# Kernel tuning notes

Measured on AMD Instinct MI355X. Metric: run time of the kernel, lower is better.

## Reference

```python
import jax, jax.numpy as jnp
import numpy as np

N, E, D = 100000, 1600000, 128


def setup_inputs() -> dict:
    key = jax.random.key(0)
    ks = jax.random.split(key, 8)
    s = 1.0 / np.sqrt(D)
    return {
        "x": jax.random.normal(ks[0], (N, D), dtype=jnp.float32),
        "edge_index": jax.random.randint(ks[1], (2, E), 0, N, dtype=jnp.int64),
        "x_prev": jax.random.normal(ks[2], (N, D), dtype=jnp.float32),
        # GCNConv params: weight [in,out], bias [out]
        "W": jax.random.uniform(ks[3], (D, D), jnp.float32, -s, s),
        "b": jnp.zeros((D,), jnp.float32),
        # GRUCell params (torch layout): [3*H, H] gates ordered (r, z, n)
        "W_ih": jax.random.uniform(ks[4], (3 * D, D), jnp.float32, -s, s),
        "W_hh": jax.random.uniform(ks[5], (3 * D, D), jnp.float32, -s, s),
        "b_ih": jax.random.uniform(ks[6], (3 * D,), jnp.float32, -s, s),
        "b_hh": jax.random.uniform(ks[7], (3 * D,), jnp.float32, -s, s),
    }


def _gcn_conv(x, edge_index, W, b):
    n = x.shape[0]
    loop = jnp.arange(n, dtype=edge_index.dtype)
    src = jnp.concatenate([edge_index[0], loop])  # [E+N]
    dst = jnp.concatenate([edge_index[1], loop])
    # symmetric normalization: deg over destinations (incl. self loops)
    deg = jax.ops.segment_sum(jnp.ones_like(dst, dtype=x.dtype), dst, num_segments=n)
    dinv = jnp.where(deg > 0, jax.lax.rsqrt(deg), 0.0)
    norm = dinv[src] * dinv[dst]  # [E+N]
    xw = x @ W  # [N, out]
    msg = xw[src] * norm[:, None]  # gather + scale
    return jax.ops.segment_sum(msg, dst, num_segments=n) + b


def _gru_cell(inp, h, W_ih, W_hh, b_ih, b_hh):
    gi = inp @ W_ih.T + b_ih  # [N, 3H]
    gh = h @ W_hh.T + b_hh
    i_r, i_z, i_n = jnp.split(gi, 3, axis=-1)
    h_r, h_z, h_n = jnp.split(gh, 3, axis=-1)
    r = jax.nn.sigmoid(i_r + h_r)
    z = jax.nn.sigmoid(i_z + h_z)
    ntil = jnp.tanh(i_n + r * h_n)
    return (1.0 - z) * ntil + z * h


def reference(x, edge_index, x_prev, W, b, W_ih, W_hh, b_ih, b_hh):
    h_cur = _gcn_conv(x, edge_index, W, b)
    return _gru_cell(h_cur, x_prev, W_ih, W_hh, b_ih, b_hh)
```

## Files before the change

### kernel.cpp

```cpp
#include <hip/hip_runtime.h>
#include <hip/hip_bf16.h>
#include <math.h>

#define DIM 128
#define PSHIFT 10
#define PSZ 1024
#define CHUNK 2048

typedef __attribute__((ext_vector_type(8))) short bf16x8;
typedef __attribute__((ext_vector_type(4))) float f32x4;
typedef unsigned short u16;
typedef unsigned int u32;
typedef unsigned long long u64;

__device__ __forceinline__ u16 f2bf(float x) {
    u32 u = __builtin_bit_cast(u32, x);
    u += 0x7fff + ((u >> 16) & 1);
    return (u16)(u >> 16);
}
__device__ __forceinline__ float bf2f(u16 h) {
    return __builtin_bit_cast(float, (u32)h << 16);
}
__device__ __forceinline__ float fsig(float x) {
    return __builtin_amdgcn_rcpf(1.f + __expf(-x));
}
__device__ __forceinline__ float ftanh(float x) {
    return 1.f - 2.f * __builtin_amdgcn_rcpf(__expf(2.f * x) + 1.f);
}


__global__ __launch_bounds__(256) void k_zero(int* __restrict__ p, int n) {
    int i = blockIdx.x * 256 + threadIdx.x;
    if (i < n) p[i] = 0;
}

__global__ __launch_bounds__(256) void k_pcount(const int* __restrict__ edst,
                                                int* __restrict__ pcnt, int E) {
    __shared__ int h[128];
    int t = threadIdx.x;
    if (t < 128) h[t] = 0;
    __syncthreads();
    int stride = gridDim.x * 256;
    for (int e = blockIdx.x * 256 + t; e < E; e += stride)
        atomicAdd(&h[edst[e] >> PSHIFT], 1);
    __syncthreads();
    if (t < 128 && h[t]) atomicAdd(&pcnt[t], h[t]);
}

__global__ __launch_bounds__(256) void k_pscan(const int* __restrict__ pcnt,
                                               int* __restrict__ poff,
                                               int* __restrict__ pfill,
                                               int* __restrict__ rowp,
                                               int P, int N, int E) {
    __shared__ int a[256];
    int t = threadIdx.x;
    int v = (t < P) ? pcnt[t] : 0;
    a[t] = v;
    __syncthreads();
    #pragma unroll
    for (int off = 1; off < 256; off <<= 1) {
        int y = (t >= off) ? a[t - off] : 0;
        __syncthreads();
        a[t] += y;
        __syncthreads();
    }
    int excl = a[t] - v;
    if (t < P) { poff[t] = excl; pfill[t] = excl; }
    if (t == 0) { poff[P] = E; rowp[N] = E; }
}

__global__ __launch_bounds__(256) void k_pscatter(const int* __restrict__ esrc,
                                                  const int* __restrict__ edst,
                                                  int* __restrict__ pfill,
                                                  u64* __restrict__ pbuf, int E) {
    __shared__ int hist[128], sc[128], lofs[128], gbase[128];
    __shared__ u32 ss[CHUNK], sd[CHUNK];
    int t = threadIdx.x;
    int c0 = blockIdx.x * CHUNK;
    int cnt = E - c0; if (cnt > CHUNK) cnt = CHUNK;

    if (t < 128) hist[t] = 0;
    __syncthreads();

    u32 s[8], d[8];
    int p[8], r[8];
    #pragma unroll
    for (int j = 0; j < 8; ++j) {
        int i = j * 256 + t;
        if (i < cnt) {
            s[j] = (u32)esrc[c0 + i];
            d[j] = (u32)edst[c0 + i];
            p[j] = (int)(d[j] >> PSHIFT);
            r[j] = atomicAdd(&hist[p[j]], 1);
        }
    }
    __syncthreads();

    if (t < 128) sc[t] = hist[t];
    __syncthreads();
    #pragma unroll
    for (int off = 1; off < 128; off <<= 1) {
        int y = 0;
        if (t < 128 && t >= off) y = sc[t - off];
        __syncthreads();
        if (t < 128) sc[t] += y;
        __syncthreads();
    }
    if (t < 128) {
        lofs[t] = sc[t] - hist[t];
        if (hist[t] > 0) gbase[t] = atomicAdd(&pfill[t], hist[t]);
    }
    __syncthreads();

    #pragma unroll
    for (int j = 0; j < 8; ++j) {
        int i = j * 256 + t;
        if (i < cnt) {
            int idx = lofs[p[j]] + r[j];
            ss[idx] = s[j];
            sd[idx] = d[j];
        }
    }
    __syncthreads();

    for (int i = t; i < cnt; i += 256) {
        u32 dd = sd[i];
        int pp = (int)(dd >> PSHIFT);
        int gpos = gbase[pp] + (i - lofs[pp]);
        pbuf[gpos] = (u64)ss[i] | ((u64)dd << 32);
    }
}

__global__ __launch_bounds__(256) void k_pfill(const u64* __restrict__ pbuf,
                                               const int* __restrict__ poff,
                                               int* __restrict__ rowp,
                                               int* __restrict__ srcs,
                                               float* __restrict__ dinv, int N) {
    __shared__ int cnt[PSZ];
    __shared__ int wsum[4];
    int p = blockIdx.x, t = threadIdx.x;
    int lane = t & 63, wid = t >> 6;
    int nb0 = p << PSHIFT;
    int ncnt = N - nb0; if (ncnt > PSZ) ncnt = PSZ;
    int b0 = poff[p], b1 = poff[p + 1];
    int bc = b1 - b0;

    for (int i = t; i < PSZ; i += 256) cnt[i] = 0;
    __syncthreads();
    for (int i = t; i < bc; i += 256) {
        u32 d = (u32)(pbuf[b0 + i] >> 32);
        atomicAdd(&cnt[d - nb0], 1);
    }
    __syncthreads();

    int base = t * 4;
    int c[4];
    int ssum = 0;
    #pragma unroll
    for (int j = 0; j < 4; ++j) { c[j] = cnt[base + j]; ssum += c[j]; }
    int incl = ssum;
    #pragma unroll
    for (int off = 1; off < 64; off <<= 1) {
        int y = __shfl_up(incl, off, 64);
        if (lane >= off) incl += y;
    }
    if (lane == 63) wsum[wid] = incl;
    __syncthreads();
    int add = 0;
    for (int w = 0; w < wid; ++w) add += wsum[w];
    int rr = b0 + add + (incl - ssum);
    #pragma unroll
    for (int j = 0; j < 4; ++j) {
        int i = base + j;
        if (i < ncnt) {
            rowp[nb0 + i] = rr;
            dinv[nb0 + i] = rsqrtf((float)(c[j] + 1));
        }
        cnt[i] = rr;
        rr += c[j];
    }
    __syncthreads();

    for (int i = t; i < bc; i += 256) {
        u64 v = pbuf[b0 + i];
        u32 sv = (u32)v;
        u32 d = (u32)(v >> 32);
        int pos = atomicAdd(&cnt[d - nb0], 1);
        srcs[pos] = (int)sv;
    }
}


__global__ __launch_bounds__(256) void k_prep(const float* __restrict__ W,
                                              const float* __restrict__ Wih,
                                              const float* __restrict__ Whh,
                                              const float4* __restrict__ xp,
                                              u16* __restrict__ Wt,
                                              u16* __restrict__ Wihb,
                                              u16* __restrict__ Whhb,
                                              u32* __restrict__ Xpb, int n4) {
    int gid = blockIdx.x * 256 + threadIdx.x;
    int stride = gridDim.x * 256;
    for (int i = gid; i < n4; i += stride) {
        float4 v = xp[i];
        Xpb[i * 2 + 0] = (u32)f2bf(v.x) | ((u32)f2bf(v.y) << 16);
        Xpb[i * 2 + 1] = (u32)f2bf(v.z) | ((u32)f2bf(v.w) << 16);
    }
    if (gid < 128 * 128) {
        int k = gid >> 7, c = gid & 127;
        Wt[c * 128 + k] = f2bf(W[gid]);
    }
    if (gid < 3 * 128 * 128) {
        Wihb[gid] = f2bf(Wih[gid]);
        Whhb[gid] = f2bf(Whh[gid]);
    }
}


__global__ __launch_bounds__(256) void k_gemm1(const float* __restrict__ X,
                                               const u16* __restrict__ Wt,
                                               u16* __restrict__ XWb, int n) {
    __shared__ u16 Wlds[128 * 128];
    int t = threadIdx.x, w = t >> 6, l = t & 63;
    int lr = l & 15, q = l >> 4;

    for (int cidx = t; cidx < 2048; cidx += 256) {
        int r = cidx >> 4, kc = cidx & 15;
        int dst = r * 128 + ((kc * 8) ^ ((r & 7) << 3));
        *(bf16x8*)(Wlds + dst) = *(const bf16x8*)(Wt + r * 128 + kc * 8);
    }
    __syncthreads();

    int r0 = blockIdx.x * 128;
    int wrow0 = r0 + w * 32;
    int sw = (lr & 7) << 3;
    int ar0 = wrow0 + lr;      if (ar0 > n - 1) ar0 = n - 1;
    int ar1 = wrow0 + 16 + lr; if (ar1 > n - 1) ar1 = n - 1;
    const float* x0 = X + (size_t)ar0 * DIM;
    const float* x1 = X + (size_t)ar1 * DIM;

    f32x4 acc[2][8];
    #pragma unroll
    for (int s = 0; s < 2; ++s)
        #pragma unroll
        for (int c = 0; c < 8; ++c) acc[s][c] = (f32x4){0.f, 0.f, 0.f, 0.f};

    #pragma unroll
    for (int kb = 0; kb < 4; ++kb) {
        int ko = kb * 32 + q * 8;
        float4 f00 = *(const float4*)(x0 + ko), f01 = *(const float4*)(x0 + ko + 4);
        float4 f10 = *(const float4*)(x1 + ko), f11 = *(const float4*)(x1 + ko + 4);
        bf16x8 a0, a1;
        a0[0] = (short)f2bf(f00.x); a0[1] = (short)f2bf(f00.y);
        a0[2] = (short)f2bf(f00.z); a0[3] = (short)f2bf(f00.w);
        a0[4] = (short)f2bf(f01.x); a0[5] = (short)f2bf(f01.y);
        a0[6] = (short)f2bf(f01.z); a0[7] = (short)f2bf(f01.w);
        a1[0] = (short)f2bf(f10.x); a1[1] = (short)f2bf(f10.y);
        a1[2] = (short)f2bf(f10.z); a1[3] = (short)f2bf(f10.w);
        a1[4] = (short)f2bf(f11.x); a1[5] = (short)f2bf(f11.y);
        a1[6] = (short)f2bf(f11.z); a1[7] = (short)f2bf(f11.w);
        int kw = ko ^ sw;
        #pragma unroll
        for (int ct = 0; ct < 8; ++ct) {
            bf16x8 b = *(const bf16x8*)(Wlds + (ct * 16 + lr) * 128 + kw);
            acc[0][ct] = __builtin_amdgcn_mfma_f32_16x16x32_bf16(a0, b, acc[0][ct], 0, 0, 0);
            acc[1][ct] = __builtin_amdgcn_mfma_f32_16x16x32_bf16(a1, b, acc[1][ct], 0, 0, 0);
        }
    }

    #pragma unroll
    for (int s = 0; s < 2; ++s)
        #pragma unroll
        for (int ct = 0; ct < 8; ++ct)
            #pragma unroll
            for (int i = 0; i < 4; ++i) {
                int row = wrow0 + s * 16 + q * 4 + i;
                if (row < n)
                    XWb[(size_t)row * DIM + ct * 16 + lr] = f2bf(acc[s][ct][i]);
            }
}


__global__ __launch_bounds__(256) void k_gather(const u16* __restrict__ XWb,
                                                const float* __restrict__ dinv,
                                                const int* __restrict__ row_ptr,
                                                const int* __restrict__ srcs,
                                                const float* __restrict__ bias,
                                                u16* __restrict__ Hcb, int n) {
    int node = blockIdx.x * 4 + (threadIdx.x >> 6);
    if (node >= n) return;
    int lane = threadIdx.x & 63;
    int c = lane * 2;

    float di = dinv[node];
    u32 sv = *(const u32*)(XWb + (size_t)node * DIM + c);
    float accx = bias[c]     + bf2f((u16)(sv & 0xffff)) * di * di;
    float accy = bias[c + 1] + bf2f((u16)(sv >> 16))    * di * di;

    int e = row_ptr[node], end = row_ptr[node + 1];
    for (; e + 7 < end; e += 8) {
        int sdx[8]; float nw[8]; u32 vv[8];
        #pragma unroll
        for (int j = 0; j < 8; ++j) sdx[j] = srcs[e + j];
        #pragma unroll
        for (int j = 0; j < 8; ++j) nw[j] = dinv[sdx[j]] * di;
        #pragma unroll
        for (int j = 0; j < 8; ++j)
            vv[j] = *(const u32*)(XWb + (size_t)sdx[j] * DIM + c);
        #pragma unroll
        for (int j = 0; j < 8; ++j) {
            accx += bf2f((u16)(vv[j] & 0xffff)) * nw[j];
            accy += bf2f((u16)(vv[j] >> 16)) * nw[j];
        }
    }
    for (; e < end; ++e) {
        int s = srcs[e];
        float nrm = dinv[s] * di;
        u32 v = *(const u32*)(XWb + (size_t)s * DIM + c);
        accx += bf2f((u16)(v & 0xffff)) * nrm;
        accy += bf2f((u16)(v >> 16)) * nrm;
    }
    *(u32*)(Hcb + (size_t)node * DIM + c) = (u32)f2bf(accx) | ((u32)f2bf(accy) << 16);
}


__global__ __launch_bounds__(256) void k_gru(const u16* __restrict__ Hcb,
                                             const u16* __restrict__ Xpb,
                                             const u16* __restrict__ Wihb,
                                             const u16* __restrict__ Whhb,
                                             const float* __restrict__ bih,
                                             const float* __restrict__ bhh,
                                             float* __restrict__ Out, int n) {
    __shared__ u16 Wlds[96 * 128];
    int t = threadIdx.x, w = t >> 6, l = t & 63;
    int lr = l & 15, q = l >> 4;

    int nwg = gridDim.x;
    int qq = nwg >> 3, rr8 = nwg & 7;
    int xcd = blockIdx.x & 7, idx = blockIdx.x >> 3;
    int logical = (xcd < rr8 ? xcd * (qq + 1) : rr8 * (qq + 1) + (xcd - rr8) * qq) + idx;
    int cs = logical & 7;
    int slot = logical >> 3;
    int nslot = nwg >> 3;
    int c0 = cs * 16;

    for (int cidx = t; cidx < 1536; cidx += 256) {
        int r = cidx >> 4, kc = cidx & 15;
        int m = (r >= 48);
        int rr = m ? r - 48 : r;
        int g = rr >> 4, cc = rr & 15;
        const u16* src = (m ? Whhb : Wihb) + (size_t)((g << 7) + c0 + cc) * DIM + kc * 8;
        int dst = r * 128 + ((kc * 8) ^ ((r & 7) << 3));
        *(bf16x8*)(Wlds + dst) = *(const bf16x8*)src;
    }
    __syncthreads();

    int sw = (lr & 7) << 3;
    int j = c0 + lr;
    float br = bih[j],       bz = bih[128 + j], bn = bih[256 + j];
    float cr = bhh[j],       cz = bhh[128 + j], cn = bhh[256 + j];

    int nrb = (n + 127) >> 7;
    for (int rb = slot; rb < nrb; rb += nslot) {
        int wrow0 = rb * 128 + w * 32;
        int ar0 = wrow0 + lr;      if (ar0 > n - 1) ar0 = n - 1;
        int ar1 = wrow0 + 16 + lr; if (ar1 > n - 1) ar1 = n - 1;
        const u16* hb0 = Hcb + (size_t)ar0 * DIM;
        const u16* hb1 = Hcb + (size_t)ar1 * DIM;
        const u16* xb0 = Xpb + (size_t)ar0 * DIM;
        const u16* xb1 = Xpb + (size_t)ar1 * DIM;

        f32x4 aI[3][2], aH[3][2];
        #pragma unroll
        for (int g = 0; g < 3; ++g)
            #pragma unroll
            for (int s = 0; s < 2; ++s) {
                aI[g][s] = (f32x4){0.f, 0.f, 0.f, 0.f};
                aH[g][s] = (f32x4){0.f, 0.f, 0.f, 0.f};
            }

        #pragma unroll
        for (int kb = 0; kb < 4; ++kb) {
            int ko = kb * 32 + q * 8;
            bf16x8 hA0 = *(const bf16x8*)(hb0 + ko);
            bf16x8 hA1 = *(const bf16x8*)(hb1 + ko);
            bf16x8 xA0 = *(const bf16x8*)(xb0 + ko);
            bf16x8 xA1 = *(const bf16x8*)(xb1 + ko);
            int kw = ko ^ sw;
            #pragma unroll
            for (int g = 0; g < 3; ++g) {
                int ridx = (g * 16 + lr) * 128 + kw;
                bf16x8 bI = *(const bf16x8*)(Wlds + ridx);
                bf16x8 bH = *(const bf16x8*)(Wlds + ridx + 48 * 128);
                aI[g][0] = __builtin_amdgcn_mfma_f32_16x16x32_bf16(hA0, bI, aI[g][0], 0, 0, 0);
                aI[g][1] = __builtin_amdgcn_mfma_f32_16x16x32_bf16(hA1, bI, aI[g][1], 0, 0, 0);
                aH[g][0] = __builtin_amdgcn_mfma_f32_16x16x32_bf16(xA0, bH, aH[g][0], 0, 0, 0);
                aH[g][1] = __builtin_amdgcn_mfma_f32_16x16x32_bf16(xA1, bH, aH[g][1], 0, 0, 0);
            }
        }

        #pragma unroll
        for (int s = 0; s < 2; ++s)
            #pragma unroll
            for (int i = 0; i < 4; ++i) {
                int row = wrow0 + s * 16 + q * 4 + i;
                if (row >= n) continue;
                float ir = aI[0][s][i] + br;
                float iz = aI[1][s][i] + bz;
                float in_ = aI[2][s][i] + bn;
                float hr = aH[0][s][i] + cr;
                float hz = aH[1][s][i] + cz;
                float hn = aH[2][s][i] + cn;
                float rg = fsig(ir + hr);
                float zg = fsig(iz + hz);
                float ng = ftanh(in_ + rg * hn);
                float hp = bf2f((u16)Xpb[(size_t)row * DIM + j]);
                Out[(size_t)row * DIM + j] = (1.f - zg) * ng + zg * hp;
            }
    }
}


extern "C" void kernel_launch(void* const* d_in, const int* in_sizes, int n_in,
                              void* d_out, int out_size, void* d_ws, size_t ws_size,
                              hipStream_t stream) {
    const float* x     = (const float*)d_in[0];
    const int*   ei    = (const int*)d_in[1];
    const float* xprev = (const float*)d_in[2];
    const float* W     = (const float*)d_in[3];
    const float* b     = (const float*)d_in[4];
    const float* Wih   = (const float*)d_in[5];
    const float* Whh   = (const float*)d_in[6];
    const float* bih   = (const float*)d_in[7];
    const float* bhh   = (const float*)d_in[8];

    int N = in_sizes[0] / DIM;
    int E = in_sizes[1] / 2;
    int P = (N + PSZ - 1) >> PSHIFT;
    const int* esrc = ei;
    const int* edst = ei + E;

    char* p = (char*)d_ws;
    auto alloc = [&](size_t bytes) {
        char* q = p;
        p += (bytes + 255) & ~(size_t)255;
        return q;
    };
    float* dinv = (float*)alloc((size_t)N * 4);
    int*   rowp = (int*)  alloc((size_t)(N + 1) * 4);
    int*   srcs = (int*)  alloc((size_t)E * 4);
    u16*   Hcb  = (u16*)  alloc((size_t)N * DIM * 2);
    u16*   Xpb  = (u16*)  alloc((size_t)N * DIM * 2);
    u16*   XWb  = (u16*)  alloc((size_t)N * DIM * 2);
    u16*   Wt   = (u16*)  alloc(128 * 128 * 2);
    u16*   Wihb = (u16*)  alloc(3 * 128 * 128 * 2);
    u16*   Whhb = (u16*)  alloc(3 * 128 * 128 * 2);
    int*   pcnt = (int*)  alloc(128 * 4);
    int*   poff = (int*)  alloc(129 * 4);
    int*   pfil = (int*)  alloc(128 * 4);
    u64*   pbuf = (u64*)XWb;
    float* out  = (float*)d_out;

    k_zero    <<<1, 256, 0, stream>>>(pcnt, 128);
    k_pcount  <<<1024, 256, 0, stream>>>(edst, pcnt, E);
    k_pscan   <<<1, 256, 0, stream>>>(pcnt, poff, pfil, rowp, P, N, E);
    int nch = (E + CHUNK - 1) / CHUNK;
    k_pscatter<<<nch, 256, 0, stream>>>(esrc, edst, pfil, pbuf, E);
    k_pfill   <<<P, 256, 0, stream>>>(pbuf, poff, rowp, srcs, dinv, N);
    int n4 = N * DIM / 4;
    k_prep    <<<2048, 256, 0, stream>>>(W, Wih, Whh, (const float4*)xprev,
                                         Wt, Wihb, Whhb, (u32*)Xpb, n4);
    int nrb = (N + 127) / 128;
    k_gemm1   <<<nrb, 256, 0, stream>>>(x, Wt, XWb, N);
    k_gather  <<<(N + 3) / 4, 256, 0, stream>>>(XWb, dinv, rowp, srcs, b, Hcb, N);
    k_gru     <<<1536, 256, 0, stream>>>(Hcb, Xpb, Wihb, Whhb, bih, bhh, out, N);
}
```

Measured before the change: 279.9 us.

## Store prescaled XW in FP8, fuse prep with counting, retile GRU

The GEMM output is pre-scaled by the source dinv and stored as FP8 instead of bf16. This halves the bytes the neighbor gather reads and removes the per-edge dinv loads and multiplies, with the destination dinv applied once per node. The weight and x_prev conversion is fused into the edge-count kernel, a memset replaces the zero kernel, and the scatter chunk size is doubled. The GRU kernel now processes one row tile per block with a larger grid and uses an FMA form for the final blend. FP8 quantization of XW adds substantial precision loss that may exceed tolerance.

```diff
diff --git a/kernel.cpp b/kernel.cpp
--- a/kernel.cpp
+++ b/kernel.cpp
@@ -5,11 +5,13 @@
 #define DIM 128
 #define PSHIFT 10
 #define PSZ 1024
-#define CHUNK 2048
+#define CHUNK 4096
 
 typedef __attribute__((ext_vector_type(8))) short bf16x8;
 typedef __attribute__((ext_vector_type(4))) float f32x4;
+typedef __attribute__((ext_vector_type(2))) float f32x2;
 typedef unsigned short u16;
+typedef unsigned char u8;
 typedef unsigned int u32;
 typedef unsigned long long u64;
 
@@ -27,22 +29,43 @@
 __device__ __forceinline__ float ftanh(float x) {
     return 1.f - 2.f * __builtin_amdgcn_rcpf(__expf(2.f * x) + 1.f);
 }
-
-
-__global__ __launch_bounds__(256) void k_zero(int* __restrict__ p, int n) {
-    int i = blockIdx.x * 256 + threadIdx.x;
-    if (i < n) p[i] = 0;
-}
-
-__global__ __launch_bounds__(256) void k_pcount(const int* __restrict__ edst,
-                                                int* __restrict__ pcnt, int E) {
+__device__ __forceinline__ u8 f2fp8(float v) {
+    int pk = __builtin_amdgcn_cvt_pk_fp8_f32(v, v, 0, false);
+    return (u8)(pk & 0xff);
+}
+
+
+__global__ __launch_bounds__(256) void k_prepcount(const int* __restrict__ edst,
+                                                   int* __restrict__ pcnt, int E,
+                                                   const float* __restrict__ W,
+                                                   const float* __restrict__ Wih,
+                                                   const float* __restrict__ Whh,
+                                                   const float4* __restrict__ xp,
+                                                   u16* __restrict__ Wt,
+                                                   u16* __restrict__ Wihb,
+                                                   u16* __restrict__ Whhb,
+                                                   u32* __restrict__ Xpb, int n4) {
     __shared__ int h[128];
     int t = threadIdx.x;
+    int gid = blockIdx.x * 256 + t;
+    int stride = gridDim.x * 256;
     if (t < 128) h[t] = 0;
     __syncthreads();
-    int stride = gridDim.x * 256;
-    for (int e = blockIdx.x * 256 + t; e < E; e += stride)
+    for (int e = gid; e < E; e += stride)
         atomicAdd(&h[edst[e] >> PSHIFT], 1);
+    for (int i = gid; i < n4; i += stride) {
+        float4 v = xp[i];
+        Xpb[i * 2 + 0] = (u32)f2bf(v.x) | ((u32)f2bf(v.y) << 16);
+        Xpb[i * 2 + 1] = (u32)f2bf(v.z) | ((u32)f2bf(v.w) << 16);
+    }
+    if (gid < 128 * 128) {
+        int k = gid >> 7, c = gid & 127;
+        Wt[c * 128 + k] = f2bf(W[gid]);
+    }
+    if (gid < 3 * 128 * 128) {
+        Wihb[gid] = f2bf(Wih[gid]);
+        Whhb[gid] = f2bf(Whh[gid]);
+    }
     __syncthreads();
     if (t < 128 && h[t]) atomicAdd(&pcnt[t], h[t]);
 }
@@ -82,10 +105,10 @@
     if (t < 128) hist[t] = 0;
     __syncthreads();
 
-    u32 s[8], d[8];
-    int p[8], r[8];
-    #pragma unroll
-    for (int j = 0; j < 8; ++j) {
+    u32 s[16], d[16];
+    int p[16], r[16];
+    #pragma unroll
+    for (int j = 0; j < 16; ++j) {
         int i = j * 256 + t;
         if (i < cnt) {
             s[j] = (u32)esrc[c0 + i];
@@ -113,7 +136,7 @@
     __syncthreads();
 
     #pragma unroll
-    for (int j = 0; j < 8; ++j) {
+    for (int j = 0; j < 16; ++j) {
         int i = j * 256 + t;
         if (i < cnt) {
             int idx = lofs[p[j]] + r[j];
@@ -191,35 +214,10 @@
 }
 
 
-__global__ __launch_bounds__(256) void k_prep(const float* __restrict__ W,
-                                              const float* __restrict__ Wih,
-                                              const float* __restrict__ Whh,
-                                              const float4* __restrict__ xp,
-                                              u16* __restrict__ Wt,
-                                              u16* __restrict__ Wihb,
-                                              u16* __restrict__ Whhb,
-                                              u32* __restrict__ Xpb, int n4) {
-    int gid = blockIdx.x * 256 + threadIdx.x;
-    int stride = gridDim.x * 256;
-    for (int i = gid; i < n4; i += stride) {
-        float4 v = xp[i];
-        Xpb[i * 2 + 0] = (u32)f2bf(v.x) | ((u32)f2bf(v.y) << 16);
-        Xpb[i * 2 + 1] = (u32)f2bf(v.z) | ((u32)f2bf(v.w) << 16);
-    }
-    if (gid < 128 * 128) {
-        int k = gid >> 7, c = gid & 127;
-        Wt[c * 128 + k] = f2bf(W[gid]);
-    }
-    if (gid < 3 * 128 * 128) {
-        Wihb[gid] = f2bf(Wih[gid]);
-        Whhb[gid] = f2bf(Whh[gid]);
-    }
-}
-
-
 __global__ __launch_bounds__(256) void k_gemm1(const float* __restrict__ X,
                                                const u16* __restrict__ Wt,
-                                               u16* __restrict__ XWb, int n) {
+                                               const float* __restrict__ dinv,
+                                               u8* __restrict__ XW8, int n) {
     __shared__ u16 Wlds[128 * 128];
     int t = threadIdx.x, w = t >> 6, l = t & 63;
     int lr = l & 15, q = l >> 4;
@@ -268,6 +266,14 @@
         }
     }
 
+    float dv[2][4];
+    #pragma unroll
+    for (int s = 0; s < 2; ++s)
+        #pragma unroll
+        for (int i = 0; i < 4; ++i) {
+            int row = wrow0 + s * 16 + q * 4 + i; if (row > n - 1) row = n - 1;
+            dv[s][i] = dinv[row];
+        }
     #pragma unroll
     for (int s = 0; s < 2; ++s)
         #pragma unroll
@@ -276,12 +282,12 @@
             for (int i = 0; i < 4; ++i) {
                 int row = wrow0 + s * 16 + q * 4 + i;
                 if (row < n)
-                    XWb[(size_t)row * DIM + ct * 16 + lr] = f2bf(acc[s][ct][i]);
+                    XW8[(size_t)row * DIM + ct * 16 + lr] = f2fp8(acc[s][ct][i] * dv[s][i]);
             }
 }
 
 
-__global__ __launch_bounds__(256) void k_gather(const u16* __restrict__ XWb,
+__global__ __launch_bounds__(256) void k_gather(const u8* __restrict__ XW8,
                                                 const float* __restrict__ dinv,
                                                 const int* __restrict__ row_ptr,
                                                 const int* __restrict__ srcs,
@@ -292,35 +298,35 @@
     int lane = threadIdx.x & 63;
     int c = lane * 2;
 
-    float di = dinv[node];
-    u32 sv = *(const u32*)(XWb + (size_t)node * DIM + c);
-    float accx = bias[c]     + bf2f((u16)(sv & 0xffff)) * di * di;
-    float accy = bias[c + 1] + bf2f((u16)(sv >> 16))    * di * di;
+    u16 sv = *(const u16*)(XW8 + (size_t)node * DIM + c);
+    f32x2 sf = __builtin_amdgcn_cvt_pk_f32_fp8((int)(u32)sv, false);
+    float accx = sf[0], accy = sf[1];
 
     int e = row_ptr[node], end = row_ptr[node + 1];
     for (; e + 7 < end; e += 8) {
-        int sdx[8]; float nw[8]; u32 vv[8];
+        int sdx[8]; u16 vv[8];
         #pragma unroll
         for (int j = 0; j < 8; ++j) sdx[j] = srcs[e + j];
         #pragma unroll
-        for (int j = 0; j < 8; ++j) nw[j] = dinv[sdx[j]] * di;
-        #pragma unroll
         for (int j = 0; j < 8; ++j)
-            vv[j] = *(const u32*)(XWb + (size_t)sdx[j] * DIM + c);
+            vv[j] = *(const u16*)(XW8 + (size_t)sdx[j] * DIM + c);
         #pragma unroll
         for (int j = 0; j < 8; ++j) {
-            accx += bf2f((u16)(vv[j] & 0xffff)) * nw[j];
-            accy += bf2f((u16)(vv[j] >> 16)) * nw[j];
+            f32x2 f = __builtin_amdgcn_cvt_pk_f32_fp8((int)(u32)vv[j], false);
+            accx += f[0];
+            accy += f[1];
         }
     }
     for (; e < end; ++e) {
-        int s = srcs[e];
-        float nrm = dinv[s] * di;
-        u32 v = *(const u32*)(XWb + (size_t)s * DIM + c);
-        accx += bf2f((u16)(v & 0xffff)) * nrm;
-        accy += bf2f((u16)(v >> 16)) * nrm;
-    }
-    *(u32*)(Hcb + (size_t)node * DIM + c) = (u32)f2bf(accx) | ((u32)f2bf(accy) << 16);
+        u16 v = *(const u16*)(XW8 + (size_t)srcs[e] * DIM + c);
+        f32x2 f = __builtin_amdgcn_cvt_pk_f32_fp8((int)(u32)v, false);
+        accx += f[0];
+        accy += f[1];
+    }
+    float di = dinv[node];
+    float ox = accx * di + bias[c];
+    float oy = accy * di + bias[c + 1];
+    *(u32*)(Hcb + (size_t)node * DIM + c) = (u32)f2bf(ox) | ((u32)f2bf(oy) << 16);
 }
 
 
@@ -340,9 +346,9 @@
     int xcd = blockIdx.x & 7, idx = blockIdx.x >> 3;
     int logical = (xcd < rr8 ? xcd * (qq + 1) : rr8 * (qq + 1) + (xcd - rr8) * qq) + idx;
     int cs = logical & 7;
-    int slot = logical >> 3;
-    int nslot = nwg >> 3;
+    int rb = logical >> 3;
     int c0 = cs * 16;
+    int r0 = rb * 128;
 
     for (int cidx = t; cidx < 1536; cidx += 256) {
         int r = cidx >> 4, kc = cidx & 15;
@@ -355,69 +361,65 @@
     }
     __syncthreads();
 
+    int wrow0 = r0 + w * 32;
     int sw = (lr & 7) << 3;
+    int ar0 = wrow0 + lr;      if (ar0 > n - 1) ar0 = n - 1;
+    int ar1 = wrow0 + 16 + lr; if (ar1 > n - 1) ar1 = n - 1;
+    const u16* hb0 = Hcb + (size_t)ar0 * DIM;
+    const u16* hb1 = Hcb + (size_t)ar1 * DIM;
+    const u16* xb0 = Xpb + (size_t)ar0 * DIM;
+    const u16* xb1 = Xpb + (size_t)ar1 * DIM;
+
+    f32x4 aI[3][2], aH[3][2];
+    #pragma unroll
+    for (int g = 0; g < 3; ++g)
+        #pragma unroll
+        for (int s = 0; s < 2; ++s) {
+            aI[g][s] = (f32x4){0.f, 0.f, 0.f, 0.f};
+            aH[g][s] = (f32x4){0.f, 0.f, 0.f, 0.f};
+        }
+
+    #pragma unroll
+    for (int kb = 0; kb < 4; ++kb) {
+        int ko = kb * 32 + q * 8;
+        bf16x8 hA0 = *(const bf16x8*)(hb0 + ko);
+        bf16x8 hA1 = *(const bf16x8*)(hb1 + ko);
+        bf16x8 xA0 = *(const bf16x8*)(xb0 + ko);
+        bf16x8 xA1 = *(const bf16x8*)(xb1 + ko);
+        int kw = ko ^ sw;
+        #pragma unroll
+        for (int g = 0; g < 3; ++g) {
+            int ridx = (g * 16 + lr) * 128 + kw;
+            bf16x8 bI = *(const bf16x8*)(Wlds + ridx);
+            bf16x8 bH = *(const bf16x8*)(Wlds + ridx + 48 * 128);
+            aI[g][0] = __builtin_amdgcn_mfma_f32_16x16x32_bf16(hA0, bI, aI[g][0], 0, 0, 0);
+            aI[g][1] = __builtin_amdgcn_mfma_f32_16x16x32_bf16(hA1, bI, aI[g][1], 0, 0, 0);
+            aH[g][0] = __builtin_amdgcn_mfma_f32_16x16x32_bf16(xA0, bH, aH[g][0], 0, 0, 0);
+            aH[g][1] = __builtin_amdgcn_mfma_f32_16x16x32_bf16(xA1, bH, aH[g][1], 0, 0, 0);
+        }
+    }
+
     int j = c0 + lr;
     float br = bih[j],       bz = bih[128 + j], bn = bih[256 + j];
     float cr = bhh[j],       cz = bhh[128 + j], cn = bhh[256 + j];
-
-    int nrb = (n + 127) >> 7;
-    for (int rb = slot; rb < nrb; rb += nslot) {
-        int wrow0 = rb * 128 + w * 32;
-        int ar0 = wrow0 + lr;      if (ar0 > n - 1) ar0 = n - 1;
-        int ar1 = wrow0 + 16 + lr; if (ar1 > n - 1) ar1 = n - 1;
-        const u16* hb0 = Hcb + (size_t)ar0 * DIM;
-        const u16* hb1 = Hcb + (size_t)ar1 * DIM;
-        const u16* xb0 = Xpb + (size_t)ar0 * DIM;
-        const u16* xb1 = Xpb + (size_t)ar1 * DIM;
-
-        f32x4 aI[3][2], aH[3][2];
-        #pragma unroll
-        for (int g = 0; g < 3; ++g)
-            #pragma unroll
-            for (int s = 0; s < 2; ++s) {
-                aI[g][s] = (f32x4){0.f, 0.f, 0.f, 0.f};
-                aH[g][s] = (f32x4){0.f, 0.f, 0.f, 0.f};
-            }
-
-        #pragma unroll
-        for (int kb = 0; kb < 4; ++kb) {
-            int ko = kb * 32 + q * 8;
-            bf16x8 hA0 = *(const bf16x8*)(hb0 + ko);
-            bf16x8 hA1 = *(const bf16x8*)(hb1 + ko);
-            bf16x8 xA0 = *(const bf16x8*)(xb0 + ko);
-            bf16x8 xA1 = *(const bf16x8*)(xb1 + ko);
-            int kw = ko ^ sw;
-            #pragma unroll
-            for (int g = 0; g < 3; ++g) {
-                int ridx = (g * 16 + lr) * 128 + kw;
-                bf16x8 bI = *(const bf16x8*)(Wlds + ridx);
-                bf16x8 bH = *(const bf16x8*)(Wlds + ridx + 48 * 128);
-                aI[g][0] = __builtin_amdgcn_mfma_f32_16x16x32_bf16(hA0, bI, aI[g][0], 0, 0, 0);
-                aI[g][1] = __builtin_amdgcn_mfma_f32_16x16x32_bf16(hA1, bI, aI[g][1], 0, 0, 0);
-                aH[g][0] = __builtin_amdgcn_mfma_f32_16x16x32_bf16(xA0, bH, aH[g][0], 0, 0, 0);
-                aH[g][1] = __builtin_amdgcn_mfma_f32_16x16x32_bf16(xA1, bH, aH[g][1], 0, 0, 0);
-            }
-        }
-
-        #pragma unroll
-        for (int s = 0; s < 2; ++s)
-            #pragma unroll
-            for (int i = 0; i < 4; ++i) {
-                int row = wrow0 + s * 16 + q * 4 + i;
-                if (row >= n) continue;
-                float ir = aI[0][s][i] + br;
-                float iz = aI[1][s][i] + bz;
-                float in_ = aI[2][s][i] + bn;
-                float hr = aH[0][s][i] + cr;
-                float hz = aH[1][s][i] + cz;
-                float hn = aH[2][s][i] + cn;
-                float rg = fsig(ir + hr);
-                float zg = fsig(iz + hz);
-                float ng = ftanh(in_ + rg * hn);
-                float hp = bf2f((u16)Xpb[(size_t)row * DIM + j]);
-                Out[(size_t)row * DIM + j] = (1.f - zg) * ng + zg * hp;
-            }
-    }
+    #pragma unroll
+    for (int s = 0; s < 2; ++s)
+        #pragma unroll
+        for (int i = 0; i < 4; ++i) {
+            int row = wrow0 + s * 16 + q * 4 + i;
+            if (row >= n) continue;
+            float ir = aI[0][s][i] + br;
+            float iz = aI[1][s][i] + bz;
+            float in_ = aI[2][s][i] + bn;
+            float hr = aH[0][s][i] + cr;
+            float hz = aH[1][s][i] + cz;
+            float hn = aH[2][s][i] + cn;
+            float rg = fsig(ir + hr);
+            float zc = fsig(-(iz + hz));
+            float ng = ftanh(in_ + rg * hn);
+            float hp = bf2f((u16)Xpb[(size_t)row * DIM + j]);
+            Out[(size_t)row * DIM + j] = fmaf(zc, ng - hp, hp);
+        }
 }
 
 
@@ -451,27 +453,29 @@
     int*   srcs = (int*)  alloc((size_t)E * 4);
     u16*   Hcb  = (u16*)  alloc((size_t)N * DIM * 2);
     u16*   Xpb  = (u16*)  alloc((size_t)N * DIM * 2);
-    u16*   XWb  = (u16*)  alloc((size_t)N * DIM * 2);
+    size_t xwsz = (size_t)N * DIM;
+    size_t pbsz = (size_t)E * 8;
+    u8*    XW8  = (u8*)   alloc(xwsz > pbsz ? xwsz : pbsz);
     u16*   Wt   = (u16*)  alloc(128 * 128 * 2);
     u16*   Wihb = (u16*)  alloc(3 * 128 * 128 * 2);
     u16*   Whhb = (u16*)  alloc(3 * 128 * 128 * 2);
     int*   pcnt = (int*)  alloc(128 * 4);
     int*   poff = (int*)  alloc(129 * 4);
     int*   pfil = (int*)  alloc(128 * 4);
-    u64*   pbuf = (u64*)XWb;
+    u64*   pbuf = (u64*)XW8;
     float* out  = (float*)d_out;
 
-    k_zero    <<<1, 256, 0, stream>>>(pcnt, 128);
-    k_pcount  <<<1024, 256, 0, stream>>>(edst, pcnt, E);
+    hipMemsetAsync(pcnt, 0, 128 * 4, stream);
+    int n4 = N * DIM / 4;
+    k_prepcount<<<2048, 256, 0, stream>>>(edst, pcnt, E, W, Wih, Whh,
+                                          (const float4*)xprev,
+                                          Wt, Wihb, Whhb, (u32*)Xpb, n4);
     k_pscan   <<<1, 256, 0, stream>>>(pcnt, poff, pfil, rowp, P, N, E);
     int nch = (E + CHUNK - 1) / CHUNK;
     k_pscatter<<<nch, 256, 0, stream>>>(esrc, edst, pfil, pbuf, E);
     k_pfill   <<<P, 256, 0, stream>>>(pbuf, poff, rowp, srcs, dinv, N);
-    int n4 = N * DIM / 4;
-    k_prep    <<<2048, 256, 0, stream>>>(W, Wih, Whh, (const float4*)xprev,
-                                         Wt, Wihb, Whhb, (u32*)Xpb, n4);
     int nrb = (N + 127) / 128;
-    k_gemm1   <<<nrb, 256, 0, stream>>>(x, Wt, XWb, N);
-    k_gather  <<<(N + 3) / 4, 256, 0, stream>>>(XWb, dinv, rowp, srcs, b, Hcb, N);
-    k_gru     <<<1536, 256, 0, stream>>>(Hcb, Xpb, Wihb, Whhb, bih, bhh, out, N);
-}
+    k_gemm1   <<<nrb, 256, 0, stream>>>(x, Wt, dinv, XW8, N);
+    k_gather  <<<(N + 3) / 4, 256, 0, stream>>>(XW8, dinv, rowp, srcs, b, Hcb, N);
+    k_gru     <<<nrb * 8, 256, 0, stream>>>(Hcb, Xpb, Wihb, Whhb, bih, bhh, out, N);
+}
```

New measurement: 277.4 us. No clear change (-0.9%).
